# Optimization experiments

Hardware: AMD Instinct MI355X
Metric: run time of the kernel (lower is better)

Reference implementation:

```python
import jax, jax.numpy as jnp
import numpy as np

B, N, D, H, KS, DQ = 2048, 20, 512, 8, 3, 64
DK = D // H
LN_EPS = 1e-5


def _conv1d_same(x_bdn, w_oik):
    # x: [B, D, N], w: [O, I, K] -> [B, O, N], 'same' padding
    return jax.lax.conv_general_dilated(
        x_bdn, w_oik, window_strides=(1,), padding='SAME',
        dimension_numbers=('NCH', 'OIH', 'NCH'))


def _layernorm(x, g, b):
    m = jnp.mean(x, axis=-1, keepdims=True)
    v = jnp.var(x, axis=-1, keepdims=True)
    return (x - m) * jax.lax.rsqrt(v + LN_EPS) * g + b


def setup_inputs() -> dict:
    key = jax.random.key(0)
    ks = jax.random.split(key, 12)
    s = 0.02
    inp = {
        'x': jax.random.normal(ks[0], (B, N, D), dtype=jnp.float32),
        'Wq': jax.random.normal(ks[1], (D, D, KS), dtype=jnp.float32) * s,
        'Wk': jax.random.normal(ks[2], (D, D, KS), dtype=jnp.float32) * s,
        'Wv': jax.random.normal(ks[3], (D, D, KS), dtype=jnp.float32) * s,
        'gq_g': jnp.ones((D,), jnp.float32), 'gq_b': jnp.zeros((D,), jnp.float32),
        'gk_g': jnp.ones((D,), jnp.float32), 'gk_b': jnp.zeros((D,), jnp.float32),
        'gv_g': jnp.ones((D,), jnp.float32), 'gv_b': jnp.zeros((D,), jnp.float32),
        'rel_table': jax.random.normal(ks[4], (2 * N - 1, H), dtype=jnp.float32) * s,
        'gsb': jax.random.normal(ks[5], (H, N, N), dtype=jnp.float32) * s,
        'alpha': jnp.asarray(1.0, jnp.float32),
        'Wqf': jax.random.normal(ks[6], (D, DQ), dtype=jnp.float32) * s,
        'bqf': jnp.zeros((DQ,), jnp.float32),
        'Wqp': jax.random.normal(ks[7], (DQ, H), dtype=jnp.float32) * s,
        'bqp': jnp.zeros((H,), jnp.float32),
        'Wo': jax.random.normal(ks[8], (D, D), dtype=jnp.float32) * s,
        'bo': jnp.zeros((D,), jnp.float32),
    }
    return inp


def reference(x, Wq, Wk, Wv, gq_g, gq_b, gk_g, gk_b, gv_g, gv_b,
              rel_table, gsb, alpha, Wqf, bqf, Wqp, bqp, Wo, bo):
    xp = jnp.transpose(x, (0, 2, 1))  # [B, D, N]
    # conv QKV projections + LayerNorm + residual (use_conv_proj=True path)
    q = x + _layernorm(jnp.transpose(_conv1d_same(xp, Wq), (0, 2, 1)), gq_g, gq_b)
    k = x + _layernorm(jnp.transpose(_conv1d_same(xp, Wk), (0, 2, 1)), gk_g, gk_b)
    v = x + _layernorm(jnp.transpose(_conv1d_same(xp, Wv), (0, 2, 1)), gv_g, gv_b)
    # split heads: [B, H, N, DK]
    q = q.reshape(B, N, H, DK).transpose(0, 2, 1, 3)
    k = k.reshape(B, N, H, DK).transpose(0, 2, 1, 3)
    v = v.reshape(B, N, H, DK).transpose(0, 2, 1, 3)
    scale = 1.0 / jnp.sqrt(jnp.asarray(DK, jnp.float32))
    scores = jnp.einsum('bhnd,bhmd->bhnm', q, k) * scale  # [B, H, N, N]
    # relative positional bias over node index
    idx = jnp.arange(N)[:, None] - jnp.arange(N)[None, :] + N - 1  # [N, N]
    rel_bias = rel_table[idx]  # [N, N, H]
    scores = scores + jnp.transpose(rel_bias, (2, 0, 1))[None]
    # learned global spatial bias
    scores = scores + alpha * gsb[None]
    # dynamic adjacency bias from pairwise node features
    qf = jnp.tanh(x @ Wqf + bqf)  # [B, N, DQ]
    pair = qf[:, :, None, :] - qf[:, None, :, :]  # [B, N, N, DQ]
    dyn = pair @ Wqp + bqp  # [B, N, N, H]
    scores = scores + jnp.transpose(dyn, (0, 3, 1, 2))
    attn = jax.nn.softmax(scores, axis=-1)
    out = jnp.einsum('bhnm,bhmd->bhnd', attn, v)
    out = out.transpose(0, 2, 1, 3).reshape(B, N, D)
    return out @ Wo + bo
```

## Files before the change

kernel.cpp:

```cpp
#include <hip/hip_runtime.h>
#include <stdint.h>

#define Bn   2048
#define Nn   20
#define Dn   512
#define Hn   8
#define Mn   (Bn*Nn)
#define K3n  1536
#define NPn  22
#define BKn  32

typedef __attribute__((ext_vector_type(4))) float  floatx4;
typedef __attribute__((ext_vector_type(8))) __bf16 bf16x8;
typedef __attribute__((ext_vector_type(4))) __bf16 bf16x4;

__device__ __forceinline__ void gload_lds16(const void* g, void* l) {
  __builtin_amdgcn_global_load_lds(
      (const __attribute__((address_space(1))) void*)g,
      (__attribute__((address_space(3))) void*)l, 16, 0, 0);
}

__global__ void k_prep_xpad(const float* __restrict__ x, __bf16* __restrict__ xpad) {
  int idx = blockIdx.x * 256 + threadIdx.x;
  int d8 = idx & 63;
  int t  = idx >> 6;
  if (t >= Bn * NPn) return;
  int n = t % NPn;
  int b = t / NPn;
  bf16x8 v;
  if (n == 0 || n == NPn - 1) {
#pragma unroll
    for (int e = 0; e < 8; ++e) v[e] = (__bf16)0.f;
  } else {
    const float4 x0 = *(const float4*)(x + (size_t)((b * Nn + n - 1) * Dn) + d8 * 8);
    const float4 x1 = *(const float4*)(x + (size_t)((b * Nn + n - 1) * Dn) + d8 * 8 + 4);
    v[0] = (__bf16)x0.x; v[1] = (__bf16)x0.y; v[2] = (__bf16)x0.z; v[3] = (__bf16)x0.w;
    v[4] = (__bf16)x1.x; v[5] = (__bf16)x1.y; v[6] = (__bf16)x1.z; v[7] = (__bf16)x1.w;
  }
  *(bf16x8*)(xpad + (size_t)t * Dn + d8 * 8) = v;
}

__global__ void k_prep_wct(const float* __restrict__ Wq, const float* __restrict__ Wk,
                           const float* __restrict__ Wv, __bf16* __restrict__ wct) {
  int idx = blockIdx.x * 256 + threadIdx.x;
  if (idx >= K3n * K3n) return;
  int kk = idx % K3n;
  int j  = idx / K3n;
  int seg = j >> 9, o = j & 511;
  int kker = kk >> 9, i = kk & 511;
  const float* W = (seg == 0) ? Wq : ((seg == 1) ? Wk : Wv);
  wct[idx] = (__bf16)W[(o * 512 + i) * 3 + kker];
}

__global__ void k_prep_wot(const float* __restrict__ Wo, __bf16* __restrict__ wot) {
  int idx = blockIdx.x * 256 + threadIdx.x;
  if (idx >= Dn * Dn) return;
  int k = idx & 511, c = idx >> 9;
  wot[idx] = (__bf16)Wo[k * Dn + c];
}

__global__ void k_prep_wqft(const float* __restrict__ Wqf, __bf16* __restrict__ wqft) {
  int idx = blockIdx.x * 256 + threadIdx.x;
  if (idx >= Dn * 64) return;
  int d = idx & 511, dq = idx >> 9;
  wqft[idx] = (__bf16)Wqf[d * 64 + dq];
}

__global__ void k_bias(const float* __restrict__ rel, const float* __restrict__ gsb,
                       const float* __restrict__ alpha, const float* __restrict__ bqp,
                       float* __restrict__ bias) {
  int idx = blockIdx.x * 256 + threadIdx.x;
  if (idx >= Hn * Nn * Nn) return;
  int j = idx % Nn;
  int i = (idx / Nn) % Nn;
  int h = idx / (Nn * Nn);
  bias[idx] = rel[(i - j + Nn - 1) * Hn + h] + alpha[0] * gsb[idx] + bqp[h];
}

__global__ __launch_bounds__(512, 2)
void k_qkv(const __bf16* __restrict__ xpad, const __bf16* __restrict__ wct,
           const float* __restrict__ gq_g, const float* __restrict__ gq_b,
           const float* __restrict__ gk_g, const float* __restrict__ gk_b,
           const float* __restrict__ gv_g, const float* __restrict__ gv_b,
           __bf16* __restrict__ qkv) {
  __shared__ __bf16 lds[3 * 20480];
  __shared__ float red1[512];
  __shared__ float red2[512];

  const int tid  = threadIdx.x;
  const int wave = tid >> 6;
  const int lane = tid & 63;
  const int quad = lane >> 4;
  const int l15  = lane & 15;
  const int rowg = wave >> 2;
  const int colg = wave & 3;

  const int bid   = blockIdx.x;
  const int xcd   = bid & 7;
  const int local = bid >> 3;
  const int seg   = local % 3;
  const int mt    = xcd * 40 + local / 3;
  const int m0    = mt * 128;

  const __bf16 *gB0, *gB1, *gB2, *gB3;
  {
    int c, col, rk;
    c = wave * 256 + 0 * 64 + lane; col = c >> 2; rk = (c & 3) ^ ((col >> 1) & 3);
    gB0 = wct + (size_t)(seg * 512 + col) * K3n + rk * 8;
    c = wave * 256 + 1 * 64 + lane; col = c >> 2; rk = (c & 3) ^ ((col >> 1) & 3);
    gB1 = wct + (size_t)(seg * 512 + col) * K3n + rk * 8;
    c = wave * 256 + 2 * 64 + lane; col = c >> 2; rk = (c & 3) ^ ((col >> 1) & 3);
    gB2 = wct + (size_t)(seg * 512 + col) * K3n + rk * 8;
    c = wave * 256 + 3 * 64 + lane; col = c >> 2; rk = (c & 3) ^ ((col >> 1) & 3);
    gB3 = wct + (size_t)(seg * 512 + col) * K3n + rk * 8;
  }
  const __bf16* gA;
  {
    int c   = tid;
    int row = c >> 2;
    int rk  = (c & 3) ^ ((row >> 1) & 3);
    int grow = m0 + row;
    int b = grow / Nn, n = grow - b * Nn;
    gA = xpad + (size_t)(b * NPn + n) * Dn + rk * 8;
  }

  int fAo0, fAo1, fAo2, fAo3, fBo[8];
  {
    int row;
    row = rowg * 64 + 0 * 16 + l15; fAo0 = row * BKn + (quad ^ ((row >> 1) & 3)) * 8;
    row = rowg * 64 + 1 * 16 + l15; fAo1 = row * BKn + (quad ^ ((row >> 1) & 3)) * 8;
    row = rowg * 64 + 2 * 16 + l15; fAo2 = row * BKn + (quad ^ ((row >> 1) & 3)) * 8;
    row = rowg * 64 + 3 * 16 + l15; fAo3 = row * BKn + (quad ^ ((row >> 1) & 3)) * 8;
#pragma unroll
    for (int tc = 0; tc < 8; ++tc) {
      int col = colg * 128 + tc * 16 + l15;
      fBo[tc] = 4096 + col * BKn + (quad ^ ((col >> 1) & 3)) * 8;
    }
  }

  const int dA = wave * 512;
  const int dB = 4096 + wave * 2048;

  floatx4 acc[4][8];
  const floatx4 zero = {0.f, 0.f, 0.f, 0.f};
#pragma unroll
  for (int i = 0; i < 4; ++i)
#pragma unroll
    for (int j = 0; j < 8; ++j) acc[i][j] = zero;

#define QKV_STAGE(NB) do {                                             \
    __bf16* _s = lds + (NB) * 20480;                                   \
    gload_lds16(gA,  _s + dA);          gA  += BKn;                    \
    gload_lds16(gB0, _s + dB);          gB0 += BKn;                    \
    gload_lds16(gB1, _s + dB + 512);    gB1 += BKn;                    \
    gload_lds16(gB2, _s + dB + 1024);   gB2 += BKn;                    \
    gload_lds16(gB3, _s + dB + 1536);   gB3 += BKn;                    \
  } while (0)

#define QKV_STEP(CB, NB, DOSTAGE, VMS) do {                            \
    if (DOSTAGE) QKV_STAGE(NB);                                        \
    const __bf16* _L = lds + (CB) * 20480;                             \
    bf16x8 _a0 = *(const bf16x8*)(_L + fAo0);                          \
    bf16x8 _a1 = *(const bf16x8*)(_L + fAo1);                          \
    bf16x8 _a2 = *(const bf16x8*)(_L + fAo2);                          \
    bf16x8 _a3 = *(const bf16x8*)(_L + fAo3);                          \
    __builtin_amdgcn_s_setprio(1);                                     \
    _Pragma("unroll")                                                  \
    for (int _n = 0; _n < 8; ++_n) {                                   \
      bf16x8 _b = *(const bf16x8*)(_L + fBo[_n]);                      \
      acc[0][_n] = __builtin_amdgcn_mfma_f32_16x16x32_bf16(_a0, _b, acc[0][_n], 0, 0, 0); \
      acc[1][_n] = __builtin_amdgcn_mfma_f32_16x16x32_bf16(_a1, _b, acc[1][_n], 0, 0, 0); \
      acc[2][_n] = __builtin_amdgcn_mfma_f32_16x16x32_bf16(_a2, _b, acc[2][_n], 0, 0, 0); \
      acc[3][_n] = __builtin_amdgcn_mfma_f32_16x16x32_bf16(_a3, _b, acc[3][_n], 0, 0, 0); \
    }                                                                  \
    __builtin_amdgcn_s_setprio(0);                                     \
    asm volatile("s_waitcnt vmcnt(" VMS ") lgkmcnt(0)\n\ts_barrier" ::: "memory"); \
  } while (0)

  QKV_STAGE(0);
  QKV_STAGE(1);
  asm volatile("s_waitcnt vmcnt(5)\n\ts_barrier" ::: "memory");

#pragma unroll 1
  for (int it = 0; it < 15; ++it) {
    QKV_STEP(0, 2, true, "5");
    QKV_STEP(1, 0, true, "5");
    QKV_STEP(2, 1, true, "5");
  }
  QKV_STEP(0, 2, true, "5");
  QKV_STEP(1, 0, false, "0");
  QKV_STEP(2, 0, false, "0");

#undef QKV_STEP
#undef QKV_STAGE

  float s1[16], s2[16];
#pragma unroll
  for (int m = 0; m < 4; ++m)
#pragma unroll
    for (int r = 0; r < 4; ++r) {
      float a = 0.f, b2 = 0.f;
#pragma unroll
      for (int n = 0; n < 8; ++n) { float v = acc[m][n][r]; a += v; b2 += v * v; }
      s1[m * 4 + r] = a; s2[m * 4 + r] = b2;
    }
#pragma unroll
  for (int off = 1; off < 16; off <<= 1)
#pragma unroll
    for (int i = 0; i < 16; ++i) {
      s1[i] += __shfl_xor(s1[i], off, 64);
      s2[i] += __shfl_xor(s2[i], off, 64);
    }
  if (l15 == 0) {
#pragma unroll
    for (int i = 0; i < 16; ++i) {
      int m = i >> 2, r = i & 3;
      int row = rowg * 64 + m * 16 + quad * 4 + r;
      red1[row * 4 + colg] = s1[i];
      red2[row * 4 + colg] = s2[i];
    }
  }
  __syncthreads();

  const float* gg = (seg == 0) ? gq_g : ((seg == 1) ? gk_g : gv_g);
  const float* bb = (seg == 0) ? gq_b : ((seg == 1) ? gk_b : gv_b);
#pragma unroll
  for (int m = 0; m < 4; ++m)
#pragma unroll
    for (int r = 0; r < 4; ++r) {
      int row = rowg * 64 + m * 16 + quad * 4 + r;
      float su = red1[row * 4] + red1[row * 4 + 1] + red1[row * 4 + 2] + red1[row * 4 + 3];
      float sq = red2[row * 4] + red2[row * 4 + 1] + red2[row * 4 + 2] + red2[row * 4 + 3];
      float mn = su * (1.f / 512.f);
      float vv = sq * (1.f / 512.f) - mn * mn;
      float rstd = rsqrtf(vv + 1e-5f);
      int grow = m0 + row;
      int b = grow / Nn, n2 = grow - b * Nn;
      const __bf16* xr = xpad + (size_t)(b * NPn + n2 + 1) * Dn;
#pragma unroll
      for (int n = 0; n < 8; ++n) {
        int col = colg * 128 + n * 16 + l15;
        float val = (acc[m][n][r] - mn) * rstd * gg[col] + bb[col] + (float)xr[col];
        qkv[(size_t)grow * K3n + seg * 512 + col] = (__bf16)val;
      }
    }
}

__global__ __launch_bounds__(256)
void k_qfqp(const __bf16* __restrict__ xpad, const __bf16* __restrict__ wqft,
            const float* __restrict__ bqf, const float* __restrict__ wqp,
            float* __restrict__ qfp) {
  __shared__ __bf16 lA[64 * BKn];
  __shared__ __bf16 lB[64 * BKn];
  __shared__ float lWqpT[8 * 64];
  const int tid  = threadIdx.x;
  const int wave = tid >> 6;
  const int lane = tid & 63;
  const int quad = lane >> 4;
  const int l15  = lane & 15;
  const int m0   = blockIdx.x * 64;

#pragma unroll
  for (int t = tid; t < 512; t += 256) {
    int col = t & 63, h = t >> 6;
    lWqpT[t] = wqp[col * 8 + h];
  }

  int c = wave * 64 + lane;
  int rowc = c >> 2;
  int rk   = (c & 3) ^ ((rowc >> 1) & 3);
  int grow = m0 + rowc;
  int b = grow / Nn, n = grow - b * Nn;
  const __bf16* gA = xpad + (size_t)(b * NPn + n + 1) * Dn + rk * 8;
  const __bf16* gB = wqft + (size_t)rowc * Dn + rk * 8;

  int frow = wave * 16 + l15;
  const __bf16* fA = lA + frow * BKn + (quad ^ ((frow >> 1) & 3)) * 8;
  const __bf16* fB[4];
#pragma unroll
  for (int tc = 0; tc < 4; ++tc) {
    int col = tc * 16 + l15;
    fB[tc] = lB + col * BKn + (quad ^ ((col >> 1) & 3)) * 8;
  }

  const floatx4 zero = {0.f, 0.f, 0.f, 0.f};
  floatx4 acc[4] = {zero, zero, zero, zero};

  for (int kt = 0; kt < Dn / BKn; ++kt) {
    gload_lds16(gA, lA + wave * 512);
    gload_lds16(gB, lB + wave * 512);
    __syncthreads();
    bf16x8 a = *(const bf16x8*)fA;
#pragma unroll
    for (int tc = 0; tc < 4; ++tc)
      acc[tc] = __builtin_amdgcn_mfma_f32_16x16x32_bf16(a, *(const bf16x8*)fB[tc], acc[tc], 0, 0, 0);
    __syncthreads();
    gA += BKn; gB += BKn;
  }

  float part[4][8];
#pragma unroll
  for (int r = 0; r < 4; ++r)
#pragma unroll
    for (int h = 0; h < 8; ++h) part[r][h] = 0.f;
#pragma unroll
  for (int tc = 0; tc < 4; ++tc) {
    int col = tc * 16 + l15;
    float bq = bqf[col];
#pragma unroll
    for (int r = 0; r < 4; ++r) {
      float t = tanhf(acc[tc][r] + bq);
#pragma unroll
      for (int h = 0; h < 8; ++h) part[r][h] += t * lWqpT[h * 64 + col];
    }
  }
#pragma unroll
  for (int off = 1; off < 16; off <<= 1)
#pragma unroll
    for (int r = 0; r < 4; ++r)
#pragma unroll
      for (int h = 0; h < 8; ++h) part[r][h] += __shfl_xor(part[r][h], off, 64);
  if (l15 == 0) {
#pragma unroll
    for (int r = 0; r < 4; ++r) {
      int row = wave * 16 + quad * 4 + r;
#pragma unroll
      for (int h = 0; h < 8; ++h)
        qfp[(size_t)(m0 + row) * 8 + h] = part[r][h];
    }
  }
}

__global__ __launch_bounds__(256)
void k_attn(const __bf16* __restrict__ qkv, const float* __restrict__ qfp,
            const float* __restrict__ bias, __bf16* __restrict__ aout) {
  __shared__ float sq[4][Nn * 64];
  __shared__ float sk[4][Nn * 68];
  __shared__ float sv[4][Nn * 68];
  __shared__ float sp[4][Nn * Nn];
  __shared__ float sf[4][Nn];
  const int tid  = threadIdx.x;
  const int w    = tid >> 6;
  const int lane = tid & 63;
  const int p0 = blockIdx.x * 4 + w;
  const int b = p0 >> 3, h = p0 & 7;
  const __bf16* qb = qkv + (size_t)b * Nn * K3n + h * 64;

  for (int idx = lane; idx < 160; idx += 64) {
    int n = idx >> 3, c = (idx & 7) * 8;
    bf16x8 qv = *(const bf16x8*)(qb + (size_t)n * K3n + c);
    bf16x8 kv = *(const bf16x8*)(qb + (size_t)n * K3n + 512 + c);
    bf16x8 vv = *(const bf16x8*)(qb + (size_t)n * K3n + 1024 + c);
#pragma unroll
    for (int e = 0; e < 8; ++e) {
      sq[w][n * 64 + c + e] = (float)qv[e];
      sk[w][n * 68 + c + e] = (float)kv[e];
      sv[w][n * 68 + c + e] = (float)vv[e];
    }
  }
  if (lane < Nn) sf[w][lane] = qfp[(size_t)(b * Nn + lane) * 8 + h];
  __syncthreads();

  const float* bh = bias + h * Nn * Nn;
  for (int p = lane; p < Nn * Nn; p += 64) {
    int i = p / Nn, j = p - i * Nn;
    const float4* q4 = (const float4*)&sq[w][i * 64];
    const float4* k4 = (const float4*)&sk[w][j * 68];
    float s = 0.f;
#pragma unroll
    for (int d4 = 0; d4 < 16; ++d4) {
      float4 qa = q4[d4], ka = k4[d4];
      s += qa.x * ka.x + qa.y * ka.y + qa.z * ka.z + qa.w * ka.w;
    }
    sp[w][p] = s * 0.125f + bh[p] + sf[w][i] - sf[w][j];
  }
  __syncthreads();
  if (lane < Nn) {
    int i = lane;
    float* row = &sp[w][i * Nn];
    float mx = row[0];
    for (int j = 1; j < Nn; ++j) mx = fmaxf(mx, row[j]);
    float sum = 0.f;
    for (int j = 0; j < Nn; ++j) { float e = __expf(row[j] - mx); row[j] = e; sum += e; }
    float inv = 1.f / sum;
    for (int j = 0; j < Nn; ++j) row[j] *= inv;
  }
  __syncthreads();
  for (int i = 0; i < Nn; ++i) {
    float a = 0.f;
#pragma unroll
    for (int j = 0; j < Nn; ++j) a += sp[w][i * Nn + j] * sv[w][j * 68 + lane];
    aout[(size_t)(b * Nn + i) * Dn + h * 64 + lane] = (__bf16)a;
  }
}

__global__ __launch_bounds__(512)
void k_oproj(const __bf16* __restrict__ aout, const __bf16* __restrict__ wot,
             const float* __restrict__ bo, float* __restrict__ out) {
  __shared__ __bf16 lA[64 * BKn];
  __shared__ __bf16 lB[512 * BKn];
  const int tid  = threadIdx.x;
  const int wave = tid >> 6;
  const int lane = tid & 63;
  const int quad = lane >> 4;
  const int l15  = lane & 15;
  const int rowg = wave >> 2;
  const int colg = wave & 3;
  const int m0   = blockIdx.x * 64;

  const __bf16* gB[4];
#pragma unroll
  for (int t = 0; t < 4; ++t) {
    int c   = wave * 256 + t * 64 + lane;
    int col = c >> 2;
    int rk  = (c & 3) ^ ((col >> 1) & 3);
    gB[t] = wot + (size_t)col * Dn + rk * 8;
  }
  const __bf16* gA;
  {
    int c   = (wave & 3) * 64 + lane;
    int row = c >> 2;
    int rk  = (c & 3) ^ ((row >> 1) & 3);
    gA = aout + (size_t)(m0 + row) * Dn + rk * 8;
  }
  const __bf16* fA[2];
#pragma unroll
  for (int tr = 0; tr < 2; ++tr) {
    int row = rowg * 32 + tr * 16 + l15;
    fA[tr] = lA + row * BKn + (quad ^ ((row >> 1) & 3)) * 8;
  }
  const __bf16* fB[8];
#pragma unroll
  for (int tc = 0; tc < 8; ++tc) {
    int col = colg * 128 + tc * 16 + l15;
    fB[tc] = lB + col * BKn + (quad ^ ((col >> 1) & 3)) * 8;
  }

  const floatx4 zero = {0.f, 0.f, 0.f, 0.f};
  floatx4 acc[2][8];
#pragma unroll
  for (int i = 0; i < 2; ++i)
#pragma unroll
    for (int j = 0; j < 8; ++j) acc[i][j] = zero;

  __bf16* dstB = lB + wave * 2048;
  __bf16* dstA = lA + (wave & 3) * 512;

  for (int kt = 0; kt < Dn / BKn; ++kt) {
#pragma unroll
    for (int t = 0; t < 4; ++t) gload_lds16(gB[t], dstB + t * 512);
    if (wave < 4) gload_lds16(gA, dstA);
    __syncthreads();
    bf16x8 a0 = *(const bf16x8*)fA[0];
    bf16x8 a1 = *(const bf16x8*)fA[1];
#pragma unroll
    for (int tc = 0; tc < 8; ++tc) {
      bf16x8 b0 = *(const bf16x8*)fB[tc];
      acc[0][tc] = __builtin_amdgcn_mfma_f32_16x16x32_bf16(a0, b0, acc[0][tc], 0, 0, 0);
      acc[1][tc] = __builtin_amdgcn_mfma_f32_16x16x32_bf16(a1, b0, acc[1][tc], 0, 0, 0);
    }
    __syncthreads();
#pragma unroll
    for (int t = 0; t < 4; ++t) gB[t] += BKn;
    gA += BKn;
  }
#pragma unroll
  for (int tr = 0; tr < 2; ++tr)
#pragma unroll
    for (int r = 0; r < 4; ++r) {
      int row = rowg * 32 + tr * 16 + quad * 4 + r;
#pragma unroll
      for (int tc = 0; tc < 8; ++tc) {
        int col = colg * 128 + tc * 16 + l15;
        out[(size_t)(m0 + row) * Dn + col] = acc[tr][tc][r] + bo[col];
      }
    }
}

static const size_t OFF_XPAD = 0;
static const size_t OFF_WCT  = 46137344;
static const size_t OFF_WOT  = 50855936;
static const size_t OFF_WQFT = 51380224;
static const size_t OFF_QKV  = 51445760;
static const size_t OFF_QFP  = 177274880;
static const size_t OFF_BIAS = 178585600;
static const size_t OFF_AOUT = 0;

extern "C" void kernel_launch(void* const* d_in, const int* in_sizes, int n_in,
                              void* d_out, int out_size, void* d_ws, size_t ws_size,
                              hipStream_t stream) {
  (void)in_sizes; (void)n_in; (void)out_size; (void)ws_size;
  const float* x     = (const float*)d_in[0];
  const float* Wq    = (const float*)d_in[1];
  const float* Wk    = (const float*)d_in[2];
  const float* Wv    = (const float*)d_in[3];
  const float* gq_g  = (const float*)d_in[4];
  const float* gq_b  = (const float*)d_in[5];
  const float* gk_g  = (const float*)d_in[6];
  const float* gk_b  = (const float*)d_in[7];
  const float* gv_g  = (const float*)d_in[8];
  const float* gv_b  = (const float*)d_in[9];
  const float* rel   = (const float*)d_in[10];
  const float* gsb   = (const float*)d_in[11];
  const float* alpha = (const float*)d_in[12];
  const float* Wqf   = (const float*)d_in[13];
  const float* bqf   = (const float*)d_in[14];
  const float* Wqp   = (const float*)d_in[15];
  const float* bqp   = (const float*)d_in[16];
  const float* Wo    = (const float*)d_in[17];
  const float* bo    = (const float*)d_in[18];
  float* out = (float*)d_out;
  char* ws = (char*)d_ws;

  __bf16* xpad = (__bf16*)(ws + OFF_XPAD);
  __bf16* wct  = (__bf16*)(ws + OFF_WCT);
  __bf16* wot  = (__bf16*)(ws + OFF_WOT);
  __bf16* wqft = (__bf16*)(ws + OFF_WQFT);
  __bf16* qkv  = (__bf16*)(ws + OFF_QKV);
  float*  qfp  = (float*)(ws + OFF_QFP);
  float*  bias = (float*)(ws + OFF_BIAS);
  __bf16* aout = (__bf16*)(ws + OFF_AOUT);

  k_prep_xpad<<<(Bn * NPn * (Dn / 8) + 255) / 256, 256, 0, stream>>>(x, xpad);
  k_prep_wct <<<(K3n * K3n + 255) / 256, 256, 0, stream>>>(Wq, Wk, Wv, wct);
  k_prep_wot <<<(Dn * Dn + 255) / 256, 256, 0, stream>>>(Wo, wot);
  k_prep_wqft<<<(Dn * 64 + 255) / 256, 256, 0, stream>>>(Wqf, wqft);
  k_bias     <<<(Hn * Nn * Nn + 255) / 256, 256, 0, stream>>>(rel, gsb, alpha, bqp, bias);

  k_qkv <<<Mn / 128 * 3, 512, 0, stream>>>(xpad, wct, gq_g, gq_b, gk_g, gk_b, gv_g, gv_b, qkv);
  k_qfqp<<<Mn / 64, 256, 0, stream>>>(xpad, wqft, bqf, Wqp, qfp);
  k_attn<<<(Bn * Hn) / 4, 256, 0, stream>>>(qkv, qfp, bias, aout);
  k_oproj<<<Mn / 64, 512, 0, stream>>>(aout, wot, bo, out);
}
```

Measured before the change: 593.5 us.

## Split QKV pipeline step into halves and reuse triple-buffered pipeline in oproj

The QKV GEMM main loop is restructured so each k-step issues B-fragment LDS reads and half of the next stage's global-to-LDS loads, then MFMAs, in two halves with extra barriers. This interleaves memory issue with compute at finer granularity. The output projection is rewritten to use the same triple-buffered 128-row tile pipeline, with a remapped block order, replacing its single-buffered 64-row loop with two syncthreads per step. The extra barriers and the larger oproj tile add synchronization and register pressure.

```diff
diff --git a/kernel.cpp b/kernel.cpp
--- a/kernel.cpp
+++ b/kernel.cpp
@@ -76,6 +76,49 @@
   int h = idx / (Nn * Nn);
   bias[idx] = rel[(i - j + Nn - 1) * Hn + h] + alpha[0] * gsb[idx] + bqp[h];
 }
+
+#define PIPE_STAGE_A(NB) do {                                          \
+    __bf16* _s = lds + (NB) * 20480;                                   \
+    gload_lds16(gA,  _s + dA);          gA  += BKn;                    \
+    gload_lds16(gB0, _s + dB);          gB0 += BKn;                    \
+    gload_lds16(gB1, _s + dB + 512);    gB1 += BKn;                    \
+  } while (0)
+#define PIPE_STAGE_B(NB) do {                                          \
+    __bf16* _s = lds + (NB) * 20480;                                   \
+    gload_lds16(gB2, _s + dB + 1024);   gB2 += BKn;                    \
+    gload_lds16(gB3, _s + dB + 1536);   gB3 += BKn;                    \
+  } while (0)
+
+#define PIPE_HALF(_L, NLO, STG) do {                                   \
+    bf16x8 _b[4];                                                      \
+    _b[0] = *(const bf16x8*)((_L) + fBo[(NLO) + 0]);                   \
+    _b[1] = *(const bf16x8*)((_L) + fBo[(NLO) + 1]);                   \
+    _b[2] = *(const bf16x8*)((_L) + fBo[(NLO) + 2]);                   \
+    _b[3] = *(const bf16x8*)((_L) + fBo[(NLO) + 3]);                   \
+    STG;                                                               \
+    asm volatile("s_barrier" ::: "memory");                            \
+    __builtin_amdgcn_s_setprio(1);                                     \
+    _Pragma("unroll")                                                  \
+    for (int _n = 0; _n < 4; ++_n) {                                   \
+      acc[0][(NLO) + _n] = __builtin_amdgcn_mfma_f32_16x16x32_bf16(_a0, _b[_n], acc[0][(NLO) + _n], 0, 0, 0); \
+      acc[1][(NLO) + _n] = __builtin_amdgcn_mfma_f32_16x16x32_bf16(_a1, _b[_n], acc[1][(NLO) + _n], 0, 0, 0); \
+      acc[2][(NLO) + _n] = __builtin_amdgcn_mfma_f32_16x16x32_bf16(_a2, _b[_n], acc[2][(NLO) + _n], 0, 0, 0); \
+      acc[3][(NLO) + _n] = __builtin_amdgcn_mfma_f32_16x16x32_bf16(_a3, _b[_n], acc[3][(NLO) + _n], 0, 0, 0); \
+    }                                                                  \
+    __builtin_amdgcn_s_setprio(0);                                     \
+  } while (0)
+
+#define PIPE_STEP(CB, NB, DOSTAGE, VMS) do {                           \
+    const __bf16* _L = lds + (CB) * 20480;                             \
+    bf16x8 _a0 = *(const bf16x8*)(_L + fAo0);                          \
+    bf16x8 _a1 = *(const bf16x8*)(_L + fAo1);                          \
+    bf16x8 _a2 = *(const bf16x8*)(_L + fAo2);                          \
+    bf16x8 _a3 = *(const bf16x8*)(_L + fAo3);                          \
+    PIPE_HALF(_L, 0, if (DOSTAGE) PIPE_STAGE_A(NB));                   \
+    asm volatile("s_barrier" ::: "memory");                            \
+    PIPE_HALF(_L, 4, if (DOSTAGE) PIPE_STAGE_B(NB));                   \
+    asm volatile("s_waitcnt vmcnt(" VMS ")\n\ts_barrier" ::: "memory");\
+  } while (0)
 
 __global__ __launch_bounds__(512, 2)
 void k_qkv(const __bf16* __restrict__ xpad, const __bf16* __restrict__ wct,
@@ -148,51 +191,19 @@
 #pragma unroll
     for (int j = 0; j < 8; ++j) acc[i][j] = zero;
 
-#define QKV_STAGE(NB) do {                                             \
-    __bf16* _s = lds + (NB) * 20480;                                   \
-    gload_lds16(gA,  _s + dA);          gA  += BKn;                    \
-    gload_lds16(gB0, _s + dB);          gB0 += BKn;                    \
-    gload_lds16(gB1, _s + dB + 512);    gB1 += BKn;                    \
-    gload_lds16(gB2, _s + dB + 1024);   gB2 += BKn;                    \
-    gload_lds16(gB3, _s + dB + 1536);   gB3 += BKn;                    \
-  } while (0)
-
-#define QKV_STEP(CB, NB, DOSTAGE, VMS) do {                            \
-    if (DOSTAGE) QKV_STAGE(NB);                                        \
-    const __bf16* _L = lds + (CB) * 20480;                             \
-    bf16x8 _a0 = *(const bf16x8*)(_L + fAo0);                          \
-    bf16x8 _a1 = *(const bf16x8*)(_L + fAo1);                          \
-    bf16x8 _a2 = *(const bf16x8*)(_L + fAo2);                          \
-    bf16x8 _a3 = *(const bf16x8*)(_L + fAo3);                          \
-    __builtin_amdgcn_s_setprio(1);                                     \
-    _Pragma("unroll")                                                  \
-    for (int _n = 0; _n < 8; ++_n) {                                   \
-      bf16x8 _b = *(const bf16x8*)(_L + fBo[_n]);                      \
-      acc[0][_n] = __builtin_amdgcn_mfma_f32_16x16x32_bf16(_a0, _b, acc[0][_n], 0, 0, 0); \
-      acc[1][_n] = __builtin_amdgcn_mfma_f32_16x16x32_bf16(_a1, _b, acc[1][_n], 0, 0, 0); \
-      acc[2][_n] = __builtin_amdgcn_mfma_f32_16x16x32_bf16(_a2, _b, acc[2][_n], 0, 0, 0); \
-      acc[3][_n] = __builtin_amdgcn_mfma_f32_16x16x32_bf16(_a3, _b, acc[3][_n], 0, 0, 0); \
-    }                                                                  \
-    __builtin_amdgcn_s_setprio(0);                                     \
-    asm volatile("s_waitcnt vmcnt(" VMS ") lgkmcnt(0)\n\ts_barrier" ::: "memory"); \
-  } while (0)
-
-  QKV_STAGE(0);
-  QKV_STAGE(1);
+  PIPE_STAGE_A(0); PIPE_STAGE_B(0);
+  PIPE_STAGE_A(1); PIPE_STAGE_B(1);
   asm volatile("s_waitcnt vmcnt(5)\n\ts_barrier" ::: "memory");
 
 #pragma unroll 1
   for (int it = 0; it < 15; ++it) {
-    QKV_STEP(0, 2, true, "5");
-    QKV_STEP(1, 0, true, "5");
-    QKV_STEP(2, 1, true, "5");
-  }
-  QKV_STEP(0, 2, true, "5");
-  QKV_STEP(1, 0, false, "0");
-  QKV_STEP(2, 0, false, "0");
-
-#undef QKV_STEP
-#undef QKV_STAGE
+    PIPE_STEP(0, 2, true, "5");
+    PIPE_STEP(1, 0, true, "5");
+    PIPE_STEP(2, 1, true, "5");
+  }
+  PIPE_STEP(0, 2, true, "5");
+  PIPE_STEP(1, 0, false, "0");
+  PIPE_STEP(2, 0, false, "0");
 
   float s1[16], s2[16];
 #pragma unroll
@@ -394,11 +405,10 @@
   }
 }
 
-__global__ __launch_bounds__(512)
+__global__ __launch_bounds__(512, 2)
 void k_oproj(const __bf16* __restrict__ aout, const __bf16* __restrict__ wot,
              const float* __restrict__ bo, float* __restrict__ out) {
-  __shared__ __bf16 lA[64 * BKn];
-  __shared__ __bf16 lB[512 * BKn];
+  __shared__ __bf16 lds[3 * 20480];
   const int tid  = threadIdx.x;
   const int wave = tid >> 6;
   const int lane = tid & 63;
@@ -406,73 +416,78 @@
   const int l15  = lane & 15;
   const int rowg = wave >> 2;
   const int colg = wave & 3;
-  const int m0   = blockIdx.x * 64;
-
-  const __bf16* gB[4];
-#pragma unroll
-  for (int t = 0; t < 4; ++t) {
-    int c   = wave * 256 + t * 64 + lane;
-    int col = c >> 2;
-    int rk  = (c & 3) ^ ((col >> 1) & 3);
-    gB[t] = wot + (size_t)col * Dn + rk * 8;
+
+  const int bid = blockIdx.x;
+  const int m0  = ((bid & 7) * 40 + (bid >> 3)) * 128;
+
+  const __bf16 *gB0, *gB1, *gB2, *gB3;
+  {
+    int c, col, rk;
+    c = wave * 256 + 0 * 64 + lane; col = c >> 2; rk = (c & 3) ^ ((col >> 1) & 3);
+    gB0 = wot + (size_t)col * Dn + rk * 8;
+    c = wave * 256 + 1 * 64 + lane; col = c >> 2; rk = (c & 3) ^ ((col >> 1) & 3);
+    gB1 = wot + (size_t)col * Dn + rk * 8;
+    c = wave * 256 + 2 * 64 + lane; col = c >> 2; rk = (c & 3) ^ ((col >> 1) & 3);
+    gB2 = wot + (size_t)col * Dn + rk * 8;
+    c = wave * 256 + 3 * 64 + lane; col = c >> 2; rk = (c & 3) ^ ((col >> 1) & 3);
+    gB3 = wot + (size_t)col * Dn + rk * 8;
   }
   const __bf16* gA;
   {
-    int c   = (wave & 3) * 64 + lane;
+    int c   = tid;
     int row = c >> 2;
     int rk  = (c & 3) ^ ((row >> 1) & 3);
     gA = aout + (size_t)(m0 + row) * Dn + rk * 8;
   }
-  const __bf16* fA[2];
-#pragma unroll
-  for (int tr = 0; tr < 2; ++tr) {
-    int row = rowg * 32 + tr * 16 + l15;
-    fA[tr] = lA + row * BKn + (quad ^ ((row >> 1) & 3)) * 8;
-  }
-  const __bf16* fB[8];
-#pragma unroll
-  for (int tc = 0; tc < 8; ++tc) {
-    int col = colg * 128 + tc * 16 + l15;
-    fB[tc] = lB + col * BKn + (quad ^ ((col >> 1) & 3)) * 8;
-  }
-
+
+  int fAo0, fAo1, fAo2, fAo3, fBo[8];
+  {
+    int row;
+    row = rowg * 64 + 0 * 16 + l15; fAo0 = row * BKn + (quad ^ ((row >> 1) & 3)) * 8;
+    row = rowg * 64 + 1 * 16 + l15; fAo1 = row * BKn + (quad ^ ((row >> 1) & 3)) * 8;
+    row = rowg * 64 + 2 * 16 + l15; fAo2 = row * BKn + (quad ^ ((row >> 1) & 3)) * 8;
+    row = rowg * 64 + 3 * 16 + l15; fAo3 = row * BKn + (quad ^ ((row >> 1) & 3)) * 8;
+#pragma unroll
+    for (int tc = 0; tc < 8; ++tc) {
+      int col = colg * 128 + tc * 16 + l15;
+      fBo[tc] = 4096 + col * BKn + (quad ^ ((col >> 1) & 3)) * 8;
+    }
+  }
+
+  const int dA = wave * 512;
+  const int dB = 4096 + wave * 2048;
+
+  floatx4 acc[4][8];
   const floatx4 zero = {0.f, 0.f, 0.f, 0.f};
-  floatx4 acc[2][8];
-#pragma unroll
-  for (int i = 0; i < 2; ++i)
+#pragma unroll
+  for (int i = 0; i < 4; ++i)
 #pragma unroll
     for (int j = 0; j < 8; ++j) acc[i][j] = zero;
 
-  __bf16* dstB = lB + wave * 2048;
-  __bf16* dstA = lA + (wave & 3) * 512;
-
-  for (int kt = 0; kt < Dn / BKn; ++kt) {
-#pragma unroll
-    for (int t = 0; t < 4; ++t) gload_lds16(gB[t], dstB + t * 512);
-    if (wave < 4) gload_lds16(gA, dstA);
-    __syncthreads();
-    bf16x8 a0 = *(const bf16x8*)fA[0];
-    bf16x8 a1 = *(const bf16x8*)fA[1];
-#pragma unroll
-    for (int tc = 0; tc < 8; ++tc) {
-      bf16x8 b0 = *(const bf16x8*)fB[tc];
-      acc[0][tc] = __builtin_amdgcn_mfma_f32_16x16x32_bf16(a0, b0, acc[0][tc], 0, 0, 0);
-      acc[1][tc] = __builtin_amdgcn_mfma_f32_16x16x32_bf16(a1, b0, acc[1][tc], 0, 0, 0);
-    }
-    __syncthreads();
-#pragma unroll
-    for (int t = 0; t < 4; ++t) gB[t] += BKn;
-    gA += BKn;
-  }
-#pragma unroll
-  for (int tr = 0; tr < 2; ++tr)
+  PIPE_STAGE_A(0); PIPE_STAGE_B(0);
+  PIPE_STAGE_A(1); PIPE_STAGE_B(1);
+  asm volatile("s_waitcnt vmcnt(5)\n\ts_barrier" ::: "memory");
+
+#pragma unroll 1
+  for (int it = 0; it < 4; ++it) {
+    PIPE_STEP(0, 2, true, "5");
+    PIPE_STEP(1, 0, true, "5");
+    PIPE_STEP(2, 1, true, "5");
+  }
+  PIPE_STEP(0, 2, true, "5");
+  PIPE_STEP(1, 0, true, "5");
+  PIPE_STEP(2, 0, false, "0");
+  PIPE_STEP(0, 0, false, "0");
+
+#pragma unroll
+  for (int m = 0; m < 4; ++m)
 #pragma unroll
     for (int r = 0; r < 4; ++r) {
-      int row = rowg * 32 + tr * 16 + quad * 4 + r;
-#pragma unroll
-      for (int tc = 0; tc < 8; ++tc) {
-        int col = colg * 128 + tc * 16 + l15;
-        out[(size_t)(m0 + row) * Dn + col] = acc[tr][tc][r] + bo[col];
+      int row = rowg * 64 + m * 16 + quad * 4 + r;
+#pragma unroll
+      for (int n = 0; n < 8; ++n) {
+        int col = colg * 128 + n * 16 + l15;
+        out[(size_t)(m0 + row) * Dn + col] = acc[m][n][r] + bo[col];
       }
     }
 }
@@ -530,5 +545,5 @@
   k_qkv <<<Mn / 128 * 3, 512, 0, stream>>>(xpad, wct, gq_g, gq_b, gk_g, gk_b, gv_g, gv_b, qkv);
   k_qfqp<<<Mn / 64, 256, 0, stream>>>(xpad, wqft, bqf, Wqp, qfp);
   k_attn<<<(Bn * Hn) / 4, 256, 0, stream>>>(qkv, qfp, bias, aout);
-  k_oproj<<<Mn / 64, 512, 0, stream>>>(aout, wot, bo, out);
-}
+  k_oproj<<<Mn / 128, 512, 0, stream>>>(aout, wot, bo, out);
+}
```

Measured after the change: 603.9 us. No clear change (+1.7%).
